# Kernel tuning notes

Hardware: AMD Instinct MI355X
Metric: run time of the kernel (lower is better)

## Reference

```python
import jax, jax.numpy as jnp
import numpy as np

D = 2          # qudit dimension
L = 22         # number of qudits; state length = D**L = 4194304
INDEX = tuple(range(L))  # rotation applied on every qudit (angle[i] indexed by qudit position)

# Generator S = Sx(j=0, k=1) on a D-level system: |0><1| + |1><0|
def _make_S():
    S = np.zeros((D, D), dtype=np.complex64)
    S[0, 1] = 1.0
    S[1, 0] = 1.0
    return jnp.asarray(S)


def setup_inputs() -> dict:
    key = jax.random.key(0)
    k1, k2, k3 = jax.random.split(key, 3)
    n = D ** L
    x_real = jax.random.normal(k1, (n,), dtype=jnp.float32)
    x_imag = jax.random.normal(k2, (n,), dtype=jnp.float32)
    angle = jax.random.uniform(k3, (L,), dtype=jnp.float32)
    return {"x_real": x_real, "x_imag": x_imag, "angle": angle}


def reference(x_real, x_imag, angle):
    # U = kron_i expm(-0.5j * angle[i] * S)  (identity on qudits not in INDEX),
    # applied as U @ x. Instead of materializing the D^L x D^L sparse unitary,
    # apply each single-qudit gate by contracting axis i of the reshaped state,
    # which is exactly the same linear map.
    S = _make_S()
    psi = (x_real + 1j * x_imag).astype(jnp.complex64).reshape((D,) * L)
    for i in range(L):
        if i in INDEX:
            M = jax.scipy.linalg.expm((-0.5j) * angle[i].astype(jnp.complex64) * S)
            # contract qudit axis i: psi'[..., a, ...] = sum_b M[a,b] psi[..., b, ...]
            psi = jnp.moveaxis(jnp.tensordot(M, psi, axes=([1], [i])), 0, i)
        # else: identity, nothing to do
    out = psi.reshape(-1)
    return jnp.stack([out.real, out.imag])  # (2, D**L) float32
```

## Files before the change

### kernel.cpp

```cpp
#include <hip/hip_runtime.h>


constexpr int NTOT = 1 << 22;

__device__ __forceinline__ void rotg(float& ar, float& ai, float& br, float& bi,
                                     float c, float s) {
    float t0 = ar, t1 = ai, t2 = br, t3 = bi;
    ar = fmaf(c, t0,  s * t3);
    ai = fmaf(c, t1, -s * t2);
    br = fmaf(c, t2,  s * t1);
    bi = fmaf(c, t3, -s * t0);
}

template<int K0, int NB>
__device__ __forceinline__ void gates(float (&ar)[16], float (&ai)[16],
                                      const float* __restrict__ ang) {
    #pragma unroll
    for (int b = 0; b < NB; ++b) {
        const int m = 1 << b;
        const float a = 0.5f * ang[21 - (K0 + b)];
        const float c = cosf(a), s = sinf(a);
        #pragma unroll
        for (int j = 0; j < 16; ++j)
            if (!(j & m)) rotg(ar[j], ai[j], ar[j | m], ai[j | m], c, s);
    }
}

__device__ __forceinline__ int slotA(int i) { return i ^ ((i >> 4) & 15); }

__global__ __launch_bounds__(1024) void rgate_low14(const float* __restrict__ xr,
                                                    const float* __restrict__ xi,
                                                    const float* __restrict__ ang,
                                                    float* __restrict__ out) {
    __shared__ float2 sv[16384];
    const int t  = threadIdx.x;
    const int g0 = blockIdx.x << 14;

    float ar[16], ai[16];
    #pragma unroll
    for (int j = 0; j < 16; ++j) {
        ar[j] = xr[g0 + t + (j << 10)];
        ai[j] = xi[g0 + t + (j << 10)];
    }

    gates<10, 4>(ar, ai, ang);
    #pragma unroll
    for (int j = 0; j < 16; ++j)
        sv[slotA(t + (j << 10))] = make_float2(ar[j], ai[j]);
    __syncthreads();

    const int base2 = (t & 63) + ((t >> 6) << 10);
    #pragma unroll
    for (int j = 0; j < 16; ++j) {
        float2 v = sv[slotA(base2 + (j << 6))];
        ar[j] = v.x; ai[j] = v.y;
    }
    gates<6, 4>(ar, ai, ang);
    #pragma unroll
    for (int j = 0; j < 16; ++j)
        sv[slotA(base2 + (j << 6))] = make_float2(ar[j], ai[j]);
    __syncthreads();

    const int base3 = (t & 3) + ((t >> 2) << 6);
    #pragma unroll
    for (int j = 0; j < 16; ++j) {
        float2 v = sv[slotA(base3 + (j << 2))];
        ar[j] = v.x; ai[j] = v.y;
    }
    gates<2, 4>(ar, ai, ang);
    #pragma unroll
    for (int j = 0; j < 16; ++j)
        sv[slotA(base3 + (j << 2))] = make_float2(ar[j], ai[j]);
    __syncthreads();

    const int base4 = t << 4;
    #pragma unroll
    for (int j = 0; j < 16; ++j) {
        float2 v = sv[slotA(base4 + j)];
        ar[j] = v.x; ai[j] = v.y;
    }
    gates<0, 2>(ar, ai, ang);
    float4* orp = (float4*)(out + g0 + base4);
    float4* oip = (float4*)(out + NTOT + g0 + base4);
    #pragma unroll
    for (int q = 0; q < 4; ++q) {
        orp[q] = make_float4(ar[4*q], ar[4*q+1], ar[4*q+2], ar[4*q+3]);
        oip[q] = make_float4(ai[4*q], ai[4*q+1], ai[4*q+2], ai[4*q+3]);
    }
}

__global__ __launch_bounds__(1024) void rgate_high8(const float* __restrict__ ang,
                                                    float* __restrict__ out) {
    __shared__ float2 sv[16384];
    const int t    = threadIdx.x;
    const int lane = t & 63, w = t >> 6;
    const int base = (blockIdx.x << 6) + lane;
    float* outr = out;
    float* outi = out + NTOT;

    float ar[16], ai[16];
    #pragma unroll
    for (int j = 0; j < 16; ++j) {
        const int g = ((j | (w << 4)) << 14) + base;
        ar[j] = outr[g]; ai[j] = outi[g];
    }

    gates<14, 4>(ar, ai, ang);
    #pragma unroll
    for (int j = 0; j < 16; ++j)
        sv[((j | (w << 4)) << 6) + lane] = make_float2(ar[j], ai[j]);
    __syncthreads();

    #pragma unroll
    for (int j = 0; j < 16; ++j) {
        float2 v = sv[((w | (j << 4)) << 6) + lane];
        ar[j] = v.x; ai[j] = v.y;
    }
    gates<18, 4>(ar, ai, ang);
    #pragma unroll
    for (int j = 0; j < 16; ++j) {
        const int g = ((w | (j << 4)) << 14) + base;
        outr[g] = ar[j]; outi[g] = ai[j];
    }
}

extern "C" void kernel_launch(void* const* d_in, const int* in_sizes, int n_in,
                              void* d_out, int out_size, void* d_ws, size_t ws_size,
                              hipStream_t stream) {
    const float* xr  = (const float*)d_in[0];
    const float* xi  = (const float*)d_in[1];
    const float* ang = (const float*)d_in[2];
    float* out = (float*)d_out;

    rgate_low14<<<256, 1024, 0, stream>>>(xr, xi, ang, out);
    rgate_high8<<<256, 1024, 0, stream>>>(ang, out);
}
```

Baseline: 116.0 us.

## Re-split qubit passes into 13+9 with 512-thread blocks and warp shuffles

Reworks the two-pass decomposition so the first kernel handles the low 13 qubits in 8K-element tiles of 512 threads, loading the input with float4 instead of strided scalars. The second kernel covers the high 9 qubits, doing one qubit via a cross-lane shuffle so shared-memory tiles shrink. Smaller blocks with a launch-bounds occupancy hint are meant to fit more blocks per CU and improve latency hiding and load coalescing. The second pass now reads 16-float contiguous segments instead of 64, which may hurt global coalescing, and block index swizzling is added.

```diff
diff --git a/kernel.cpp b/kernel.cpp
--- a/kernel.cpp
+++ b/kernel.cpp
@@ -12,12 +12,12 @@
     bi = fmaf(c, t3, -s * t0);
 }
 
-template<int K0, int NB>
-__device__ __forceinline__ void gates(float (&ar)[16], float (&ai)[16],
-                                      const float* __restrict__ ang) {
+template<int K0, int NB, int MSH>
+__device__ __forceinline__ void gatesM(float (&ar)[16], float (&ai)[16],
+                                       const float* __restrict__ ang) {
     #pragma unroll
     for (int b = 0; b < NB; ++b) {
-        const int m = 1 << b;
+        const int m = 1 << (MSH + b);
         const float a = 0.5f * ang[21 - (K0 + b)];
         const float c = cosf(a), s = sinf(a);
         #pragma unroll
@@ -28,98 +28,121 @@
 
 __device__ __forceinline__ int slotA(int i) { return i ^ ((i >> 4) & 15); }
 
-__global__ __launch_bounds__(1024) void rgate_low14(const float* __restrict__ xr,
-                                                    const float* __restrict__ xi,
-                                                    const float* __restrict__ ang,
-                                                    float* __restrict__ out) {
-    __shared__ float2 sv[16384];
+__global__ __launch_bounds__(512, 4) void rgate_A(const float* __restrict__ xr,
+                                                  const float* __restrict__ xi,
+                                                  const float* __restrict__ ang,
+                                                  float* __restrict__ out) {
+    __shared__ float2 sv[8192];
     const int t  = threadIdx.x;
-    const int g0 = blockIdx.x << 14;
+    const int g0 = blockIdx.x << 13;
 
     float ar[16], ai[16];
     #pragma unroll
+    for (int q = 0; q < 4; ++q) {
+        const int i = (t << 2) + (q << 11);
+        float4 vr = *(const float4*)(xr + g0 + i);
+        float4 vi = *(const float4*)(xi + g0 + i);
+        ar[4*q+0] = vr.x; ar[4*q+1] = vr.y; ar[4*q+2] = vr.z; ar[4*q+3] = vr.w;
+        ai[4*q+0] = vi.x; ai[4*q+1] = vi.y; ai[4*q+2] = vi.z; ai[4*q+3] = vi.w;
+    }
+    gatesM<11, 2, 2>(ar, ai, ang);
+
+    #pragma unroll
+    for (int q = 0; q < 4; ++q)
+        #pragma unroll
+        for (int r = 0; r < 4; ++r)
+            sv[slotA((t << 2) + r + (q << 11))] = make_float2(ar[4*q+r], ai[4*q+r]);
+    __syncthreads();
+
+    const int b2 = (t & 3) + ((t >> 2) << 6);
+    #pragma unroll
     for (int j = 0; j < 16; ++j) {
-        ar[j] = xr[g0 + t + (j << 10)];
-        ai[j] = xi[g0 + t + (j << 10)];
+        float2 v = sv[slotA(b2 + (j << 2))];
+        ar[j] = v.x; ai[j] = v.y;
     }
-
-    gates<10, 4>(ar, ai, ang);
+    gatesM<2, 4, 0>(ar, ai, ang);
     #pragma unroll
     for (int j = 0; j < 16; ++j)
-        sv[slotA(t + (j << 10))] = make_float2(ar[j], ai[j]);
+        sv[slotA(b2 + (j << 2))] = make_float2(ar[j], ai[j]);
     __syncthreads();
 
-    const int base2 = (t & 63) + ((t >> 6) << 10);
+    const int b3 = (t & 63) + ((t >> 6) << 10);
     #pragma unroll
     for (int j = 0; j < 16; ++j) {
-        float2 v = sv[slotA(base2 + (j << 6))];
+        float2 v = sv[slotA(b3 + (j << 6))];
         ar[j] = v.x; ai[j] = v.y;
     }
-    gates<6, 4>(ar, ai, ang);
+    gatesM<6, 4, 0>(ar, ai, ang);
     #pragma unroll
     for (int j = 0; j < 16; ++j)
-        sv[slotA(base2 + (j << 6))] = make_float2(ar[j], ai[j]);
+        sv[slotA(b3 + (j << 6))] = make_float2(ar[j], ai[j]);
     __syncthreads();
 
-    const int base3 = (t & 3) + ((t >> 2) << 6);
+    const int b4 = ((t & 255) << 2) + ((t >> 8) << 12);
     #pragma unroll
-    for (int j = 0; j < 16; ++j) {
-        float2 v = sv[slotA(base3 + (j << 2))];
-        ar[j] = v.x; ai[j] = v.y;
-    }
-    gates<2, 4>(ar, ai, ang);
-    #pragma unroll
-    for (int j = 0; j < 16; ++j)
-        sv[slotA(base3 + (j << 2))] = make_float2(ar[j], ai[j]);
-    __syncthreads();
+    for (int q = 0; q < 4; ++q)
+        #pragma unroll
+        for (int r = 0; r < 4; ++r) {
+            float2 v = sv[slotA(b4 + r + (q << 10))];
+            ar[4*q+r] = v.x; ai[4*q+r] = v.y;
+        }
+    gatesM<0, 2, 0>(ar, ai, ang);
+    gatesM<10, 1, 2>(ar, ai, ang);
 
-    const int base4 = t << 4;
-    #pragma unroll
-    for (int j = 0; j < 16; ++j) {
-        float2 v = sv[slotA(base4 + j)];
-        ar[j] = v.x; ai[j] = v.y;
-    }
-    gates<0, 2>(ar, ai, ang);
-    float4* orp = (float4*)(out + g0 + base4);
-    float4* oip = (float4*)(out + NTOT + g0 + base4);
     #pragma unroll
     for (int q = 0; q < 4; ++q) {
-        orp[q] = make_float4(ar[4*q], ar[4*q+1], ar[4*q+2], ar[4*q+3]);
-        oip[q] = make_float4(ai[4*q], ai[4*q+1], ai[4*q+2], ai[4*q+3]);
+        const int i = b4 + (q << 10);
+        *(float4*)(out + g0 + i)        = make_float4(ar[4*q], ar[4*q+1], ar[4*q+2], ar[4*q+3]);
+        *(float4*)(out + NTOT + g0 + i) = make_float4(ai[4*q], ai[4*q+1], ai[4*q+2], ai[4*q+3]);
     }
 }
 
-__global__ __launch_bounds__(1024) void rgate_high8(const float* __restrict__ ang,
-                                                    float* __restrict__ out) {
-    __shared__ float2 sv[16384];
-    const int t    = threadIdx.x;
-    const int lane = t & 63, w = t >> 6;
-    const int base = (blockIdx.x << 6) + lane;
+__global__ __launch_bounds__(512, 4) void rgate_B(const float* __restrict__ ang,
+                                                  float* __restrict__ out) {
+    __shared__ float2 sv[8192];
+    const int t   = threadIdx.x;
+    const int bid = blockIdx.x;
+    const int blk = (bid >> 3) | ((bid & 7) << 6);
+    const int sub = t & 15, hw = t >> 4;
+    const int lbase = (blk << 4) + sub;
     float* outr = out;
     float* outi = out + NTOT;
 
     float ar[16], ai[16];
     #pragma unroll
     for (int j = 0; j < 16; ++j) {
-        const int g = ((j | (w << 4)) << 14) + base;
+        const int g = ((j | (hw << 4)) << 13) + lbase;
         ar[j] = outr[g]; ai[j] = outi[g];
     }
+    gatesM<13, 4, 0>(ar, ai, ang);
 
-    gates<14, 4>(ar, ai, ang);
+    {
+        const float a = 0.5f * ang[21 - 17];
+        const float c = cosf(a), s = sinf(a);
+        #pragma unroll
+        for (int j = 0; j < 16; ++j) {
+            float pr = __shfl_xor(ar[j], 16, 64);
+            float pi = __shfl_xor(ai[j], 16, 64);
+            ar[j] = fmaf(c, ar[j],  s * pi);
+            ai[j] = fmaf(c, ai[j], -s * pr);
+        }
+    }
+
     #pragma unroll
     for (int j = 0; j < 16; ++j)
-        sv[((j | (w << 4)) << 6) + lane] = make_float2(ar[j], ai[j]);
+        sv[((j | (hw << 4)) << 4) + sub] = make_float2(ar[j], ai[j]);
     __syncthreads();
 
     #pragma unroll
     for (int j = 0; j < 16; ++j) {
-        float2 v = sv[((w | (j << 4)) << 6) + lane];
+        float2 v = sv[((hw | (j << 5)) << 4) + sub];
         ar[j] = v.x; ai[j] = v.y;
     }
-    gates<18, 4>(ar, ai, ang);
+    gatesM<18, 4, 0>(ar, ai, ang);
+
     #pragma unroll
     for (int j = 0; j < 16; ++j) {
-        const int g = ((w | (j << 4)) << 14) + base;
+        const int g = ((hw | (j << 5)) << 13) + lbase;
         outr[g] = ar[j]; outi[g] = ai[j];
     }
 }
@@ -132,6 +155,6 @@
     const float* ang = (const float*)d_in[2];
     float* out = (float*)d_out;
 
-    rgate_low14<<<256, 1024, 0, stream>>>(xr, xi, ang, out);
-    rgate_high8<<<256, 1024, 0, stream>>>(ang, out);
+    rgate_A<<<512, 512, 0, stream>>>(xr, xi, ang, out);
+    rgate_B<<<512, 512, 0, stream>>>(ang, out);
 }
```

Measured after the change: 106.5 us, median of 2. 8.2% less time.
